# Kernel optimization log

Hardware: AMD Instinct MI355X
Metric: run time of the kernel (lower is better)

The kernel has to match this reference:

```python
import jax, jax.numpy as jnp
import numpy as np

DIMS = 3; B = 256; N = 256; K = 16; HID = 64; INC = 64; F = 64; EPG = 8192; DEPTH = 3
EPS = 1e-15


def setup_inputs() -> dict:
    key = jax.random.key(0)
    ks = jax.random.split(key, 16)
    E = B * EPG
    g = jnp.repeat(jnp.arange(B), EPG)
    row = (g * N + jax.random.randint(ks[0], (E,), 0, N)).astype(jnp.int32)
    col = (g * N + jax.random.randint(ks[1], (E,), 0, N)).astype(jnp.int32)
    edge_index = jnp.stack([row, col])
    edge_attr = jax.random.uniform(ks[2], (E, DIMS), dtype=jnp.float32)
    x = jax.random.normal(ks[3], (B * N, INC), dtype=jnp.float32)
    x_to_pool = jax.random.normal(ks[4], (B * N, F * DIMS), dtype=jnp.float32)
    batch = jnp.repeat(jnp.arange(B), N).astype(jnp.int32)
    def w(k, shape, fan):
        return (jax.random.normal(k, shape, dtype=jnp.float32) / np.float32(np.sqrt(fan)))
    return dict(
        x=x, edge_attr=edge_attr, x_to_pool=x_to_pool,
        Wm0=w(ks[5], (DIMS, INC, HID), INC), Ws0=w(ks[6], (DIMS, INC, HID), INC), b0=jnp.zeros((DIMS, HID), jnp.float32),
        Wm1=w(ks[7], (DIMS, HID, HID), HID), Ws1=w(ks[8], (DIMS, HID, HID), HID), b1=jnp.zeros((DIMS, HID), jnp.float32),
        Wm2=w(ks[9], (DIMS, HID, K), HID), Ws2=w(ks[10], (DIMS, HID, K), HID), b2=jnp.zeros((DIMS, K), jnp.float32),
        fcW1=w(ks[11], (HID * (DEPTH - 1) + K, 50), HID * (DEPTH - 1) + K), fcb1=jnp.zeros((50,), jnp.float32),
        fcW2=w(ks[12], (50, K), 50), fcb2=jnp.zeros((K,), jnp.float32),
        edge_index=edge_index, batch=batch,
    )


def reference(x, edge_attr, x_to_pool, Wm0, Ws0, b0, Wm1, Ws1, b1, Wm2, Ws2, b2,
              fcW1, fcb1, fcW2, fcb2, edge_index, batch):
    row, col = edge_index[0], edge_index[1]
    n_total = B * N

    # ---- batch_to_adj: scatter edge list into dense (dims, B, N, N) adjacency ----
    ge, rl, cl = row // N, row % N, col % N
    adj = jnp.zeros((DIMS, B, N, N), x.dtype).at[:, ge, rl, cl].add(edge_attr.T)

    # ---- ParallelResGraphConv: per-dim edge-weighted graph conv stack ----
    def gconv(h, we, Wm, Ws, b):
        agg = jax.ops.segment_sum(we[:, None] * h[col], row, num_segments=n_total)
        return jax.nn.relu(agg @ Wm + h @ Ws + b)

    assignments = []
    for d in range(DIMS):  # small fixed loop over parallel streams
        we = edge_attr[:, d]
        h0 = gconv(x, we, Wm0[d], Ws0[d], b0[d])
        h1 = gconv(h0, we, Wm1[d], Ws1[d], b1[d])
        h2 = gconv(h1, we, Wm2[d], Ws2[d], b2[d])
        conv_out = jnp.concatenate([h0, h1, h2], axis=-1)  # [BN, HID*2+K]
        logits = (conv_out @ fcW1 + fcb1) @ fcW2 + fcb2     # shared pool_fc
        assignments.append(logits)
    s = jax.nn.softmax(jnp.stack(assignments).reshape(DIMS, B, N, K), axis=-1)

    # ---- losses: modularity (edge gather) + entropy ----
    a_flat = s.reshape(DIMS, n_total, K)
    mod = jnp.float32(0.0)
    for d in range(DIMS):
        diff = a_flat[d, row] - a_flat[d, col]
        mod = mod + jnp.mean(edge_attr[:, d] * jnp.sum(diff * diff, axis=-1))
    ent = jnp.mean(jnp.sum(-s * jnp.log(s + EPS), axis=-1))
    loss = mod + ent

    # ---- DiffPool-style pooling ----
    xr = x_to_pool.reshape(n_total, F, DIMS)
    xr = jnp.transpose(xr, (2, 0, 1)).reshape(DIMS, B, N, F)
    px = jnp.einsum('dbnk,dbnf->dbkf', s, xr)
    tmp = jnp.einsum('dbnk,dbnm->dbkm', s, adj)
    padj = jnp.einsum('dbkm,dbml->dbkl', tmp, s)
    scale = jnp.float32(K / N)
    px = jnp.transpose(px, (1, 2, 3, 0)).reshape(B * K, F, DIMS) * scale
    padj = padj * (scale * scale)

    # ---- adj_to_tg_batch: dense pooled adjacency back to edge list (fixed shapes) ----
    rows = jnp.repeat(jnp.arange(K), K)
    cols = jnp.tile(jnp.arange(K), K)
    off = (jnp.arange(B) * K)[:, None]
    pei = jnp.stack([(off + rows[None, :]).reshape(-1), (off + cols[None, :]).reshape(-1)]).astype(jnp.int32)
    pea = jax.lax.stop_gradient(jnp.transpose(padj, (1, 2, 3, 0)).reshape(-1, DIMS))  # detach_pool=True
    pbatch = jnp.repeat(jnp.arange(B), K).astype(jnp.int32)
    return (px, pei, pea, pbatch, loss, s)
```

## Files before the change

### kernel.cpp

```cpp
#include <hip/hip_runtime.h>

#define DIMS 3
#define NB 256
#define NN 256
#define KK 16
#define HID 64
#define EPG 8192
#define NTOT (NB*NN)
#define NE (NB*EPG)

#define PX_OFF   0
#define PEI_OFF  786432
#define PEA_OFF  917504
#define PB_OFF   1114112
#define LOSS_OFF 1118208
#define S_OFF    1118209

#define WREC_WS  0
#define CLREC_WS 25165824
#define IPTR_WS  27262976
#define ENT_WS   27526144
#define MOD_WS   27529216
#define WC_WS    27532288
#define BC_WS    27541504

__global__ void fc_combine(const float* __restrict__ fcW1, const float* __restrict__ fcb1,
                           const float* __restrict__ fcW2, const float* __restrict__ fcb2,
                           float* __restrict__ wc, float* __restrict__ bc)
{
    const int t = threadIdx.x;
    for (int idx = t; idx < 144 * 16; idx += 256) {
        const int i = idx >> 4, k = idx & 15;
        float s = 0.f;
        for (int q = 0; q < 50; ++q) s += fcW1[i * 50 + q] * fcW2[q * 16 + k];
        wc[idx] = s;
    }
    if (t < 16) {
        float s = fcb2[t];
        for (int q = 0; q < 50; ++q) s += fcb1[q] * fcW2[q * 16 + t];
        bc[t] = s;
    }
}

#define HSTR 132
#define PSTR 129
__launch_bounds__(256)
__global__ void csr_build(const int* __restrict__ edge_index,
                          const float* __restrict__ edge_attr,
                          float* __restrict__ wrec, unsigned char* __restrict__ clrec,
                          int* __restrict__ indptr)
{
    __shared__ unsigned char  h[256 * HSTR];
    __shared__ unsigned short po[256 * PSTR];
    __shared__ int sc[256];
    const int b = blockIdx.x;
    const int t = threadIdx.x;
    const int* rowp = edge_index + (size_t)b * EPG;
    const int* colp = edge_index + (size_t)NB * EPG + (size_t)b * EPG;

    for (int i = t; i < 256 * HSTR / 4; i += 256) ((unsigned int*)h)[i] = 0u;
    __syncthreads();

    if (t < 128) {
        #pragma unroll 4
        for (int j = 0; j < 64; ++j) {
            const int r = rowp[t + 128 * j] & (NN - 1);
            h[r * HSTR + t]++;
        }
    }
    __syncthreads();

    int tot;
    {
        int s = 0;
        const unsigned int* hr = (const unsigned int*)(h + t * HSTR);
        #pragma unroll
        for (int c4 = 0; c4 < HSTR / 4; ++c4) {
            const unsigned int v = hr[c4];
            s += (v & 255) + ((v >> 8) & 255) + ((v >> 16) & 255) + (v >> 24);
        }
        tot = s;
        sc[t] = s;
    }
    __syncthreads();
    for (int ofs = 1; ofs < 256; ofs <<= 1) {
        int v = (t >= ofs) ? sc[t - ofs] : 0;
        __syncthreads();
        sc[t] += v;
        __syncthreads();
    }
    const int start = sc[t] - tot;
    indptr[b * 257 + t] = start;
    if (t == 255) indptr[b * 257 + 256] = EPG;

    {
        int run = start;
        #pragma unroll 4
        for (int c = 0; c < 128; ++c) {
            po[t * PSTR + c] = (unsigned short)run;
            run += h[t * HSTR + c];
        }
    }
    __syncthreads();

    if (t < 128) {
        const float* eap = edge_attr + (size_t)b * EPG * 3;
        float* w0 = wrec + (size_t)b * EPG;
        float* w1 = wrec + (size_t)NB * EPG + (size_t)b * EPG;
        float* w2 = wrec + 2 * (size_t)NB * EPG + (size_t)b * EPG;
        unsigned char* cdst = clrec + (size_t)b * EPG;
        #pragma unroll 2
        for (int j = 0; j < 64; ++j) {
            const int e = t + 128 * j;
            const int r = rowp[e] & (NN - 1);
            const int cl = colp[e] & (NN - 1);
            const int dest = po[r * PSTR + t]++;
            w0[dest] = eap[e * 3 + 0];
            w1[dest] = eap[e * 3 + 1];
            w2[dest] = eap[e * 3 + 2];
            cdst[dest] = (unsigned char)cl;
        }
    }
}

template<int OUTW, bool IS_L2>
__device__ __forceinline__ void layer_step(
    int rp, int o, int fr, int fkq, int js0, int je0, int je1,
    const float* __restrict__ wp, const unsigned char* __restrict__ clp,
    const float* __restrict__ Wm, const float* __restrict__ Ws,
    const float* __restrict__ bias, const float* __restrict__ wc,
    float4* hb4, float* p)
{
    constexpr int NCO = OUTW / 8;
    const int r0 = rp * 2, r1 = r0 + 1;
    const int b0 = r0 * 16, s0 = r0 & 15;
    const int b1 = r1 * 16, s1 = r1 & 15;
    const int c0 = o, c1 = o + 8;

    float ga0[8], ga1[8];
    #pragma unroll
    for (int u = 0; u < 8; ++u) { ga0[u] = 0.f; ga1[u] = 0.f; }
    for (int j = js0; j < je0; ++j) {
        const int cl = clp[j];
        const float w = wp[j];
        const int cb = cl * 16, cs = cl & 15;
        const float4 ha = hb4[cb + (c0 ^ cs)];
        const float4 hb = hb4[cb + (c1 ^ cs)];
        ga0[0] += w * ha.x; ga0[1] += w * ha.y; ga0[2] += w * ha.z; ga0[3] += w * ha.w;
        ga0[4] += w * hb.x; ga0[5] += w * hb.y; ga0[6] += w * hb.z; ga0[7] += w * hb.w;
    }
    for (int j = je0; j < je1; ++j) {
        const int cl = clp[j];
        const float w = wp[j];
        const int cb = cl * 16, cs = cl & 15;
        const float4 ha = hb4[cb + (c0 ^ cs)];
        const float4 hb = hb4[cb + (c1 ^ cs)];
        ga1[0] += w * ha.x; ga1[1] += w * ha.y; ga1[2] += w * ha.z; ga1[3] += w * ha.w;
        ga1[4] += w * hb.x; ga1[5] += w * hb.y; ga1[6] += w * hb.z; ga1[7] += w * hb.w;
    }

    const int jA = o * 4;
    const int jB = o * 4 + 32;
    const int j0L2 = o * NCO;
    float acc0[NCO == 8 ? 8 : 2], acc1[NCO == 8 ? 8 : 2];
    if constexpr (NCO == 8) {
        const float4 bv0 = *(const float4*)(bias + jA);
        const float4 bv1 = *(const float4*)(bias + jB);
        acc0[0]=bv0.x; acc0[1]=bv0.y; acc0[2]=bv0.z; acc0[3]=bv0.w;
        acc0[4]=bv1.x; acc0[5]=bv1.y; acc0[6]=bv1.z; acc0[7]=bv1.w;
        #pragma unroll
        for (int u = 0; u < 8; ++u) acc1[u] = acc0[u];
    } else {
        acc0[0] = bias[j0L2]; acc0[1] = bias[j0L2 + 1];
        acc1[0] = acc0[0];    acc1[1] = acc0[1];
    }
    #pragma unroll 1
    for (int ic = 0; ic < 16; ++ic) {
        const float4 h40 = hb4[b0 + (ic ^ s0)];
        const float4 h41 = hb4[b1 + (ic ^ s1)];
        const float hv0[4] = {h40.x, h40.y, h40.z, h40.w};
        const float hv1[4] = {h41.x, h41.y, h41.z, h41.w};
        #pragma unroll
        for (int u = 0; u < 4; ++u) {
            const float* wr = Ws + (ic * 4 + u) * OUTW;
            const float a0 = hv0[u], a1 = hv1[u];
            if constexpr (NCO == 8) {
                const float4 wa = *(const float4*)(wr + jA);
                const float4 wb = *(const float4*)(wr + jB);
                acc0[0]+=a0*wa.x; acc0[1]+=a0*wa.y; acc0[2]+=a0*wa.z; acc0[3]+=a0*wa.w;
                acc0[4]+=a0*wb.x; acc0[5]+=a0*wb.y; acc0[6]+=a0*wb.z; acc0[7]+=a0*wb.w;
                acc1[0]+=a1*wa.x; acc1[1]+=a1*wa.y; acc1[2]+=a1*wa.z; acc1[3]+=a1*wa.w;
                acc1[4]+=a1*wb.x; acc1[5]+=a1*wb.y; acc1[6]+=a1*wb.z; acc1[7]+=a1*wb.w;
            } else {
                const float2 w2 = *(const float2*)(wr + j0L2);
                acc0[0]+=a0*w2.x; acc0[1]+=a0*w2.y;
                acc1[0]+=a1*w2.x; acc1[1]+=a1*w2.y;
            }
        }
    }
    __syncthreads();

    {
        float4 v;
        v.x = ga0[0]; v.y = ga0[1]; v.z = ga0[2]; v.w = ga0[3]; hb4[b0 + (c0 ^ s0)] = v;
        v.x = ga0[4]; v.y = ga0[5]; v.z = ga0[6]; v.w = ga0[7]; hb4[b0 + (c1 ^ s0)] = v;
        v.x = ga1[0]; v.y = ga1[1]; v.z = ga1[2]; v.w = ga1[3]; hb4[b1 + (c0 ^ s1)] = v;
        v.x = ga1[4]; v.y = ga1[5]; v.z = ga1[6]; v.w = ga1[7]; hb4[b1 + (c1 ^ s1)] = v;
    }
    __syncthreads();

    #pragma unroll 1
    for (int ic = 0; ic < 16; ++ic) {
        const float4 a40 = hb4[b0 + (ic ^ s0)];
        const float4 a41 = hb4[b1 + (ic ^ s1)];
        const float av0[4] = {a40.x, a40.y, a40.z, a40.w};
        const float av1[4] = {a41.x, a41.y, a41.z, a41.w};
        #pragma unroll
        for (int u = 0; u < 4; ++u) {
            const float* wr = Wm + (ic * 4 + u) * OUTW;
            const float a0 = av0[u], a1 = av1[u];
            if constexpr (NCO == 8) {
                const float4 wa = *(const float4*)(wr + jA);
                const float4 wb = *(const float4*)(wr + jB);
                acc0[0]+=a0*wa.x; acc0[1]+=a0*wa.y; acc0[2]+=a0*wa.z; acc0[3]+=a0*wa.w;
                acc0[4]+=a0*wb.x; acc0[5]+=a0*wb.y; acc0[6]+=a0*wb.z; acc0[7]+=a0*wb.w;
                acc1[0]+=a1*wa.x; acc1[1]+=a1*wa.y; acc1[2]+=a1*wa.z; acc1[3]+=a1*wa.w;
                acc1[4]+=a1*wb.x; acc1[5]+=a1*wb.y; acc1[6]+=a1*wb.z; acc1[7]+=a1*wb.w;
            } else {
                const float2 w2 = *(const float2*)(wr + j0L2);
                acc0[0]+=a0*w2.x; acc0[1]+=a0*w2.y;
                acc1[0]+=a1*w2.x; acc1[1]+=a1*w2.y;
            }
        }
    }
    #pragma unroll
    for (int jj = 0; jj < NCO; ++jj) {
        acc0[jj] = fmaxf(acc0[jj], 0.f);
        acc1[jj] = fmaxf(acc1[jj], 0.f);
    }
    __syncthreads();

    if constexpr (!IS_L2) {
        float4 v;
        v.x = acc0[0]; v.y = acc0[1]; v.z = acc0[2]; v.w = acc0[3]; hb4[b0 + (c0 ^ s0)] = v;
        v.x = acc0[4]; v.y = acc0[5]; v.z = acc0[6]; v.w = acc0[7]; hb4[b0 + (c1 ^ s0)] = v;
        v.x = acc1[0]; v.y = acc1[1]; v.z = acc1[2]; v.w = acc1[3]; hb4[b1 + (c0 ^ s1)] = v;
        v.x = acc1[4]; v.y = acc1[5]; v.z = acc1[6]; v.w = acc1[7]; hb4[b1 + (c1 ^ s1)] = v;
    } else {
        float* hbf = (float*)hb4;
        const int cc = o >> 1, off = (o & 1) * 2;
        float* p0 = hbf + (b0 + (cc ^ s0)) * 4 + off;
        float* p1 = hbf + (b1 + (cc ^ s1)) * 4 + off;
        p0[0] = acc0[0]; p0[1] = acc0[1];
        p1[0] = acc1[0]; p1[1] = acc1[1];
    }
    __syncthreads();

    {
        const int rb = fr * 16, rs = fr & 15;
        if constexpr (!IS_L2) {
            #pragma unroll 2
            for (int c4 = 0; c4 < 16; ++c4) {
                const float4 v4 = hb4[rb + (c4 ^ rs)];
                const float vv[4] = {v4.x, v4.y, v4.z, v4.w};
                #pragma unroll
                for (int e = 0; e < 4; ++e) {
                    const float4 w4 = *(const float4*)(wc + (c4 * 4 + e) * 16 + fkq * 4);
                    p[0] += vv[e] * w4.x; p[1] += vv[e] * w4.y;
                    p[2] += vv[e] * w4.z; p[3] += vv[e] * w4.w;
                }
            }
        } else {
            #pragma unroll 2
            for (int c4 = 0; c4 < 4; ++c4) {
                const float4 v4 = hb4[rb + (c4 ^ rs)];
                const float vv[4] = {v4.x, v4.y, v4.z, v4.w};
                #pragma unroll
                for (int e = 0; e < 4; ++e) {
                    const float4 w4 = *(const float4*)(wc + (c4 * 4 + e) * 16 + fkq * 4);
                    p[0] += vv[e] * w4.x; p[1] += vv[e] * w4.y;
                    p[2] += vv[e] * w4.z; p[3] += vv[e] * w4.w;
                }
            }
        }
    }
}

__launch_bounds__(1024)
__global__ void gconv_kernel(
    const float* __restrict__ x,
    const float* __restrict__ Wm0, const float* __restrict__ Ws0, const float* __restrict__ b0,
    const float* __restrict__ Wm1, const float* __restrict__ Ws1, const float* __restrict__ b1,
    const float* __restrict__ Wm2, const float* __restrict__ Ws2, const float* __restrict__ b2,
    const float* __restrict__ wcomb, const float* __restrict__ bcomb,
    const float* __restrict__ wrec, const unsigned char* __restrict__ clrec,
    const int* __restrict__ indptr,
    float* __restrict__ out, float* __restrict__ entpart)
{
    __shared__ float4 hb4[4096];
    __shared__ float  red[16];
    const int t = threadIdx.x;
    const int bid = blockIdx.x;
    const int d = bid >> 8;
    const int b = bid & (NB - 1);
    const int rp = t >> 3;
    const int o = t & 7;
    const int fr = t >> 2;
    const int fkq = t & 3;
    const int lane = t & 63;
    const int wave = t >> 6;

    {
        const float4* xv = (const float4*)(x + (size_t)b * NN * HID);
        #pragma unroll
        for (int it = 0; it < 4; ++it) {
            const int idx = t + it * 1024;
            const int nrow = idx >> 4, c = idx & 15;
            hb4[nrow * 16 + (c ^ (nrow & 15))] = xv[idx];
        }
    }
    float p[4] = {0.f, 0.f, 0.f, 0.f};
    __syncthreads();

    const float* wp = wrec + (size_t)d * NB * EPG + (size_t)b * EPG;
    const unsigned char* clp = clrec + (size_t)b * EPG;
    const int js0 = indptr[b * 257 + rp * 2];
    const int je0 = indptr[b * 257 + rp * 2 + 1];
    const int je1 = indptr[b * 257 + rp * 2 + 2];

    layer_step<64, false>(rp, o, fr, fkq, js0, je0, je1, wp, clp, Wm0 + d*HID*HID,
                          Ws0 + d*HID*HID, b0 + d*HID, wcomb,          hb4, p);
    layer_step<64, false>(rp, o, fr, fkq, js0, je0, je1, wp, clp, Wm1 + d*HID*HID,
                          Ws1 + d*HID*HID, b1 + d*HID, wcomb + 64*16,  hb4, p);
    layer_step<16, true >(rp, o, fr, fkq, js0, je0, je1, wp, clp, Wm2 + d*HID*KK,
                          Ws2 + d*HID*KK,  b2 + d*KK,  wcomb + 128*16, hb4, p);

    __syncthreads();
    {
        float* hbf = (float*)hb4;
        float* dst = hbf + fr * 17 + fkq * 4;
        dst[0] = p[0]; dst[1] = p[1]; dst[2] = p[2]; dst[3] = p[3];
    }
    __syncthreads();

    float ent_local = 0.f;
    if (t < 256) {
        const int rr = t;
        const float* Lr = (const float*)hb4 + rr * 17;
        float logits[KK];
        #pragma unroll
        for (int k = 0; k < KK; ++k) logits[k] = Lr[k] + bcomb[k];
        float m = logits[0];
        #pragma unroll
        for (int k = 1; k < KK; ++k) m = fmaxf(m, logits[k]);
        float sum = 0.f, sv[KK];
        #pragma unroll
        for (int k = 0; k < KK; ++k) { sv[k] = expf(logits[k] - m); sum += sv[k]; }
        const float inv = 1.f / sum;
        float4* sp4 = (float4*)(out + S_OFF + ((size_t)(d * NB + b) * NN + rr) * KK);
        #pragma unroll
        for (int q4 = 0; q4 < 4; ++q4) {
            float4 v;
            const float s0 = sv[q4*4+0] * inv, s1 = sv[q4*4+1] * inv;
            const float s2 = sv[q4*4+2] * inv, s3 = sv[q4*4+3] * inv;
            v.x = s0; v.y = s1; v.z = s2; v.w = s3;
            sp4[q4] = v;
            ent_local -= s0 * logf(s0 + 1e-15f) + s1 * logf(s1 + 1e-15f)
                       + s2 * logf(s2 + 1e-15f) + s3 * logf(s3 + 1e-15f);
        }
    }
    #pragma unroll
    for (int off = 32; off; off >>= 1) ent_local += __shfl_down(ent_local, off);
    if (lane == 0) red[wave] = ent_local;
    __syncthreads();
    if (t == 0) {
        float s = 0.f;
        #pragma unroll
        for (int w = 0; w < 16; ++w) s += red[w];
        entpart[bid] = s;
    }
}

#define SSTR 20
__launch_bounds__(256)
__global__ void pool_kernel(
    const float* __restrict__ x_to_pool,
    const float* __restrict__ wrec, const unsigned char* __restrict__ clrec,
    const int* __restrict__ indptr,
    const float* __restrict__ out_s, float* __restrict__ out, float* __restrict__ modpart)
{
    __shared__ float sl[NN * SSTR];
    __shared__ float gl[NN * SSTR];
    __shared__ float padjw[4 * 256];
    __shared__ float red[4];
    const int t = threadIdx.x;
    const int bid = blockIdx.x;
    const int d = bid >> 8;
    const int b = bid & (NB - 1);
    const int lane = t & 63;
    const int wave = t >> 6;

    {
        const float4* sp4 = (const float4*)(out_s + S_OFF + (size_t)(d * NB + b) * NN * KK);
        #pragma unroll
        for (int it = 0; it < 4; ++it) {
            const int idx = t + it * 256;
            const int nrow = idx >> 2, c = idx & 3;
            *(float4*)(sl + nrow * SSTR + c * 4) = sp4[idx];
        }
    }
    __syncthreads();

    const float* wp = wrec + (size_t)d * NB * EPG + (size_t)b * EPG;
    const unsigned char* clp = clrec + (size_t)b * EPG;
    const int js = indptr[b * 257 + t];
    const int je = indptr[b * 257 + t + 1];
    float sr[16];
    {
        #pragma unroll
        for (int c = 0; c < 4; ++c) {
            const float4 v = *(const float4*)(sl + t * SSTR + c * 4);
            sr[c*4+0] = v.x; sr[c*4+1] = v.y; sr[c*4+2] = v.z; sr[c*4+3] = v.w;
        }
    }
    float g[16];
    #pragma unroll
    for (int k = 0; k < 16; ++k) g[k] = 0.f;
    float modacc = 0.f;
    for (int j = js; j < je; ++j) {
        const int cl = clp[j];
        const float w = wp[j];
        const float* srow = sl + cl * SSTR;
        float ss = 0.f;
        #pragma unroll
        for (int c = 0; c < 4; ++c) {
            const float4 sv = *(const float4*)(srow + c * 4);
            g[c*4+0] += w * sv.x; g[c*4+1] += w * sv.y;
            g[c*4+2] += w * sv.z; g[c*4+3] += w * sv.w;
            const float d0 = sr[c*4+0] - sv.x, d1 = sr[c*4+1] - sv.y;
            const float d2 = sr[c*4+2] - sv.z, d3 = sr[c*4+3] - sv.w;
            ss += d0*d0 + d1*d1 + d2*d2 + d3*d3;
        }
        modacc += w * ss;
    }
    {
        #pragma unroll
        for (int c = 0; c < 4; ++c) {
            float4 v; v.x = g[c*4+0]; v.y = g[c*4+1]; v.z = g[c*4+2]; v.w = g[c*4+3];
            *(float4*)(gl + t * SSTR + c * 4) = v;
        }
    }
    __syncthreads();

    {
        const int k = t & 15, lg = (t >> 4) & 3;
        float p0 = 0.f, p1 = 0.f, p2 = 0.f, p3 = 0.f;
        const int r0 = wave * 64;
        for (int rr = r0; rr < r0 + 64; ++rr) {
            const float sk = sl[rr * SSTR + k];
            const float4 g4 = *(const float4*)(gl + rr * SSTR + lg * 4);
            p0 += sk * g4.x; p1 += sk * g4.y; p2 += sk * g4.z; p3 += sk * g4.w;
        }
        float* pw = padjw + wave * 256 + k * 16 + lg * 4;
        pw[0] = p0; pw[1] = p1; pw[2] = p2; pw[3] = p3;
    }

    {
        const int f = t & 63;
        const int kg = t >> 6;
        float xa0 = 0.f, xa1 = 0.f, xa2 = 0.f, xa3 = 0.f;
        const float* xp = x_to_pool + (size_t)b * NN * (64 * DIMS) + f * DIMS + d;
        #pragma unroll 4
        for (int nn2 = 0; nn2 < NN; ++nn2) {
            const float xv = xp[(size_t)nn2 * (64 * DIMS)];
            const float4 s4 = *(const float4*)(sl + nn2 * SSTR + kg * 4);
            xa0 += xv * s4.x; xa1 += xv * s4.y; xa2 += xv * s4.z; xa3 += xv * s4.w;
        }
        const float sc = 1.f / 16.f;
        out[PX_OFF + ((size_t)((b * KK + kg * 4 + 0) * 64) + f) * DIMS + d] = xa0 * sc;
        out[PX_OFF + ((size_t)((b * KK + kg * 4 + 1) * 64) + f) * DIMS + d] = xa1 * sc;
        out[PX_OFF + ((size_t)((b * KK + kg * 4 + 2) * 64) + f) * DIMS + d] = xa2 * sc;
        out[PX_OFF + ((size_t)((b * KK + kg * 4 + 3) * 64) + f) * DIMS + d] = xa3 * sc;
    }

    #pragma unroll
    for (int off = 32; off; off >>= 1) modacc += __shfl_down(modacc, off);
    if (lane == 0) red[wave] = modacc;
    __syncthreads();
    if (t == 0) modpart[bid] = red[0] + red[1] + red[2] + red[3];

    {
        const float v = (padjw[t] + padjw[256 + t] + padjw[512 + t] + padjw[768 + t]) * (1.f / 256.f);
        out[PEA_OFF + (size_t)((b * KK + (t >> 4)) * KK + (t & 15)) * DIMS + d] = v;
    }
}

__global__ void aux_kernel(float* __restrict__ out)
{
    const int idx = blockIdx.x * 256 + threadIdx.x;
    if (idx < 2 * NTOT) {
        const int r = idx & (NTOT - 1);
        const int bb = r >> 8;
        const int j = r & 255;
        const int v = (idx < NTOT) ? (bb * KK + (j >> 4)) : (bb * KK + (j & 15));
        out[PEI_OFF + idx] = (float)v;
    } else if (idx < 2 * NTOT + NB * KK) {
        const int i = idx - 2 * NTOT;
        out[PB_OFF + i] = (float)(i >> 4);
    }
}

__global__ void loss_kernel(const float* __restrict__ entpart,
                            const float* __restrict__ modpart,
                            float* __restrict__ out)
{
    const int tid = threadIdx.x;
    float e = 0.f, m = 0.f;
    for (int i = tid; i < DIMS * NB; i += 256) { e += entpart[i]; m += modpart[i]; }
    #pragma unroll
    for (int off = 32; off; off >>= 1) { e += __shfl_down(e, off); m += __shfl_down(m, off); }
    __shared__ float er[4], mr[4];
    const int wave = tid >> 6, lane = tid & 63;
    if (lane == 0) { er[wave] = e; mr[wave] = m; }
    __syncthreads();
    if (tid == 0) {
        const float es = er[0] + er[1] + er[2] + er[3];
        const float ms = mr[0] + mr[1] + mr[2] + mr[3];
        out[LOSS_OFF] = ms / (float)NE + es / (float)(DIMS * NTOT);
    }
}

extern "C" void kernel_launch(void* const* d_in, const int* in_sizes, int n_in,
                              void* d_out, int out_size, void* d_ws, size_t ws_size,
                              hipStream_t stream)
{
    const float* x         = (const float*)d_in[0];
    const float* edge_attr = (const float*)d_in[1];
    const float* x_to_pool = (const float*)d_in[2];
    const float* Wm0 = (const float*)d_in[3];
    const float* Ws0 = (const float*)d_in[4];
    const float* b0  = (const float*)d_in[5];
    const float* Wm1 = (const float*)d_in[6];
    const float* Ws1 = (const float*)d_in[7];
    const float* b1  = (const float*)d_in[8];
    const float* Wm2 = (const float*)d_in[9];
    const float* Ws2 = (const float*)d_in[10];
    const float* b2  = (const float*)d_in[11];
    const float* fcW1= (const float*)d_in[12];
    const float* fcb1= (const float*)d_in[13];
    const float* fcW2= (const float*)d_in[14];
    const float* fcb2= (const float*)d_in[15];
    const int* edge_index = (const int*)d_in[16];
    float* out = (float*)d_out;
    char* ws = (char*)d_ws;
    float*         wrec  = (float*)(ws + WREC_WS);
    unsigned char* clrec = (unsigned char*)(ws + CLREC_WS);
    int*           iptr  = (int*)(ws + IPTR_WS);
    float*         entpart = (float*)(ws + ENT_WS);
    float*         modpart = (float*)(ws + MOD_WS);
    float*         wc    = (float*)(ws + WC_WS);
    float*         bc    = (float*)(ws + BC_WS);

    csr_build<<<dim3(NB), dim3(256), 0, stream>>>(edge_index, edge_attr, wrec, clrec, iptr);
    fc_combine<<<dim3(1), dim3(256), 0, stream>>>(fcW1, fcb1, fcW2, fcb2, wc, bc);
    gconv_kernel<<<dim3(DIMS * NB), dim3(1024), 0, stream>>>(
        x, Wm0, Ws0, b0, Wm1, Ws1, b1, Wm2, Ws2, b2,
        wc, bc, wrec, clrec, iptr, out, entpart);
    pool_kernel<<<dim3(DIMS * NB), dim3(256), 0, stream>>>(
        x_to_pool, wrec, clrec, iptr, out, out, modpart);
    aux_kernel<<<dim3((2 * NTOT + NB * KK + 255) / 256), dim3(256), 0, stream>>>(out);
    loss_kernel<<<dim3(1), dim3(256), 0, stream>>>(entpart, modpart, out);
}
```

Before: 578.8 us.

## Fuse pooling stage into gconv kernel, keeping assignments in shared memory

The separate pool_kernel is folded into the tail of gconv_kernel. The softmax assignments are kept in LDS instead of being re-read from global memory, and the pooling work is redistributed across 1024 threads. Aggregation now uses 4 threads per row, padj uses 4 row groups, and the px reduction is split into 4 row groups combined through shared memory. This removes a kernel launch and a global round trip of s. The cost is extra work and barriers at the end of a high-occupancy 1024-thread kernel.

Measured after the change: 575.6 us. Within noise of the previous version (-0.6%).

```diff
diff --git a/kernel.cpp b/kernel.cpp
--- a/kernel.cpp
+++ b/kernel.cpp
@@ -23,6 +23,13 @@
 #define MOD_WS   27529216
 #define WC_WS    27532288
 #define BC_WS    27541504
+
+#define SL_OFF   0
+#define GL_OFF   5120
+#define PXP_OFF  10240
+#define PJW_OFF  14336
+#define MRED_OFF 15360
+#define ERED_OFF 15380
 
 __global__ void fc_combine(const float* __restrict__ fcW1, const float* __restrict__ fcb1,
                            const float* __restrict__ fcW2, const float* __restrict__ fcb2,
@@ -289,16 +296,17 @@
 __launch_bounds__(1024)
 __global__ void gconv_kernel(
     const float* __restrict__ x,
+    const float* __restrict__ x_to_pool,
     const float* __restrict__ Wm0, const float* __restrict__ Ws0, const float* __restrict__ b0,
     const float* __restrict__ Wm1, const float* __restrict__ Ws1, const float* __restrict__ b1,
     const float* __restrict__ Wm2, const float* __restrict__ Ws2, const float* __restrict__ b2,
     const float* __restrict__ wcomb, const float* __restrict__ bcomb,
     const float* __restrict__ wrec, const unsigned char* __restrict__ clrec,
     const int* __restrict__ indptr,
-    float* __restrict__ out, float* __restrict__ entpart)
+    float* __restrict__ out, float* __restrict__ entpart, float* __restrict__ modpart)
 {
     __shared__ float4 hb4[4096];
-    __shared__ float  red[16];
+    float* hbf = (float*)hb4;
     const int t = threadIdx.x;
     const int bid = blockIdx.x;
     const int d = bid >> 8;
@@ -324,9 +332,10 @@
 
     const float* wp = wrec + (size_t)d * NB * EPG + (size_t)b * EPG;
     const unsigned char* clp = clrec + (size_t)b * EPG;
-    const int js0 = indptr[b * 257 + rp * 2];
-    const int je0 = indptr[b * 257 + rp * 2 + 1];
-    const int je1 = indptr[b * 257 + rp * 2 + 2];
+    const int* ipb = indptr + b * 257;
+    const int js0 = ipb[rp * 2];
+    const int je0 = ipb[rp * 2 + 1];
+    const int je1 = ipb[rp * 2 + 2];
 
     layer_step<64, false>(rp, o, fr, fkq, js0, je0, je1, wp, clp, Wm0 + d*HID*HID,
                           Ws0 + d*HID*HID, b0 + d*HID, wcomb,          hb4, p);
@@ -337,8 +346,7 @@
 
     __syncthreads();
     {
-        float* hbf = (float*)hb4;
-        float* dst = hbf + fr * 17 + fkq * 4;
+        float* dst = hbf + SL_OFF + fr * 20 + fkq * 4;
         dst[0] = p[0]; dst[1] = p[1]; dst[2] = p[2]; dst[3] = p[3];
     }
     __syncthreads();
@@ -346,7 +354,7 @@
     float ent_local = 0.f;
     if (t < 256) {
         const int rr = t;
-        const float* Lr = (const float*)hb4 + rr * 17;
+        float* Lr = hbf + SL_OFF + rr * 20;
         float logits[KK];
         #pragma unroll
         for (int k = 0; k < KK; ++k) logits[k] = Lr[k] + bcomb[k];
@@ -365,133 +373,91 @@
             const float s2 = sv[q4*4+2] * inv, s3 = sv[q4*4+3] * inv;
             v.x = s0; v.y = s1; v.z = s2; v.w = s3;
             sp4[q4] = v;
+            *(float4*)(Lr + q4 * 4) = v;
             ent_local -= s0 * logf(s0 + 1e-15f) + s1 * logf(s1 + 1e-15f)
                        + s2 * logf(s2 + 1e-15f) + s3 * logf(s3 + 1e-15f);
         }
     }
     #pragma unroll
     for (int off = 32; off; off >>= 1) ent_local += __shfl_down(ent_local, off);
-    if (lane == 0) red[wave] = ent_local;
+    if (lane == 0) hbf[ERED_OFF + wave] = ent_local;
     __syncthreads();
     if (t == 0) {
         float s = 0.f;
         #pragma unroll
-        for (int w = 0; w < 16; ++w) s += red[w];
+        for (int w = 0; w < 16; ++w) s += hbf[ERED_OFF + w];
         entpart[bid] = s;
     }
-}
-
-#define SSTR 20
-__launch_bounds__(256)
-__global__ void pool_kernel(
-    const float* __restrict__ x_to_pool,
-    const float* __restrict__ wrec, const unsigned char* __restrict__ clrec,
-    const int* __restrict__ indptr,
-    const float* __restrict__ out_s, float* __restrict__ out, float* __restrict__ modpart)
-{
-    __shared__ float sl[NN * SSTR];
-    __shared__ float gl[NN * SSTR];
-    __shared__ float padjw[4 * 256];
-    __shared__ float red[4];
-    const int t = threadIdx.x;
-    const int bid = blockIdx.x;
-    const int d = bid >> 8;
-    const int b = bid & (NB - 1);
-    const int lane = t & 63;
-    const int wave = t >> 6;
-
-    {
-        const float4* sp4 = (const float4*)(out_s + S_OFF + (size_t)(d * NB + b) * NN * KK);
-        #pragma unroll
-        for (int it = 0; it < 4; ++it) {
-            const int idx = t + it * 256;
-            const int nrow = idx >> 2, c = idx & 3;
-            *(float4*)(sl + nrow * SSTR + c * 4) = sp4[idx];
-        }
-    }
-    __syncthreads();
-
-    const float* wp = wrec + (size_t)d * NB * EPG + (size_t)b * EPG;
-    const unsigned char* clp = clrec + (size_t)b * EPG;
-    const int js = indptr[b * 257 + t];
-    const int je = indptr[b * 257 + t + 1];
-    float sr[16];
-    {
-        #pragma unroll
-        for (int c = 0; c < 4; ++c) {
-            const float4 v = *(const float4*)(sl + t * SSTR + c * 4);
-            sr[c*4+0] = v.x; sr[c*4+1] = v.y; sr[c*4+2] = v.z; sr[c*4+3] = v.w;
-        }
-    }
-    float g[16];
-    #pragma unroll
-    for (int k = 0; k < 16; ++k) g[k] = 0.f;
-    float modacc = 0.f;
-    for (int j = js; j < je; ++j) {
-        const int cl = clp[j];
-        const float w = wp[j];
-        const float* srow = sl + cl * SSTR;
-        float ss = 0.f;
-        #pragma unroll
-        for (int c = 0; c < 4; ++c) {
-            const float4 sv = *(const float4*)(srow + c * 4);
-            g[c*4+0] += w * sv.x; g[c*4+1] += w * sv.y;
-            g[c*4+2] += w * sv.z; g[c*4+3] += w * sv.w;
-            const float d0 = sr[c*4+0] - sv.x, d1 = sr[c*4+1] - sv.y;
-            const float d2 = sr[c*4+2] - sv.z, d3 = sr[c*4+3] - sv.w;
-            ss += d0*d0 + d1*d1 + d2*d2 + d3*d3;
-        }
-        modacc += w * ss;
-    }
-    {
-        #pragma unroll
-        for (int c = 0; c < 4; ++c) {
-            float4 v; v.x = g[c*4+0]; v.y = g[c*4+1]; v.z = g[c*4+2]; v.w = g[c*4+3];
-            *(float4*)(gl + t * SSTR + c * 4) = v;
-        }
-    }
-    __syncthreads();
-
-    {
-        const int k = t & 15, lg = (t >> 4) & 3;
-        float p0 = 0.f, p1 = 0.f, p2 = 0.f, p3 = 0.f;
-        const int r0 = wave * 64;
-        for (int rr = r0; rr < r0 + 64; ++rr) {
-            const float sk = sl[rr * SSTR + k];
-            const float4 g4 = *(const float4*)(gl + rr * SSTR + lg * 4);
-            p0 += sk * g4.x; p1 += sk * g4.y; p2 += sk * g4.z; p3 += sk * g4.w;
-        }
-        float* pw = padjw + wave * 256 + k * 16 + lg * 4;
-        pw[0] = p0; pw[1] = p1; pw[2] = p2; pw[3] = p3;
-    }
-
-    {
-        const int f = t & 63;
-        const int kg = t >> 6;
+
+    {
+        const int pr = t >> 2, pkq = t & 3;
+        const int pjs = ipb[pr], pje = ipb[pr + 1];
+        const float4 sq = *(const float4*)(hbf + SL_OFF + pr * 20 + pkq * 4);
+        float g0 = 0.f, g1 = 0.f, g2 = 0.f, g3 = 0.f;
+        float modp = 0.f;
+        for (int j = pjs; j < pje; ++j) {
+            const int cl = clp[j];
+            const float w = wp[j];
+            const float4 sc4 = *(const float4*)(hbf + SL_OFF + cl * 20 + pkq * 4);
+            g0 += w * sc4.x; g1 += w * sc4.y; g2 += w * sc4.z; g3 += w * sc4.w;
+            const float d0 = sq.x - sc4.x, d1 = sq.y - sc4.y;
+            const float d2 = sq.z - sc4.z, d3 = sq.w - sc4.w;
+            modp += w * (d0*d0 + d1*d1 + d2*d2 + d3*d3);
+        }
+        float4 gv; gv.x = g0; gv.y = g1; gv.z = g2; gv.w = g3;
+        *(float4*)(hbf + GL_OFF + pr * 20 + pkq * 4) = gv;
+        #pragma unroll
+        for (int off = 32; off; off >>= 1) modp += __shfl_down(modp, off);
+        if (lane == 0) hbf[MRED_OFF + wave] = modp;
+    }
+    __syncthreads();
+    if (t == 0) {
+        float s = 0.f;
+        #pragma unroll
+        for (int w = 0; w < 16; ++w) s += hbf[MRED_OFF + w];
+        modpart[bid] = s;
+    }
+
+    {
+        const int q = t >> 8, kl = t & 255;
+        const int k = kl >> 4, l = kl & 15;
+        float acc = 0.f;
+        const int r0 = q * 64;
+        #pragma unroll 4
+        for (int r = r0; r < r0 + 64; ++r)
+            acc += hbf[SL_OFF + r * 20 + k] * hbf[GL_OFF + r * 20 + l];
+        hbf[PJW_OFF + q * 256 + kl] = acc;
+    }
+
+    {
+        const int rg = t >> 8, kg = (t >> 6) & 3, f = t & 63;
+        const float* xp = x_to_pool + (size_t)b * NN * (64 * DIMS) + f * DIMS + d;
         float xa0 = 0.f, xa1 = 0.f, xa2 = 0.f, xa3 = 0.f;
-        const float* xp = x_to_pool + (size_t)b * NN * (64 * DIMS) + f * DIMS + d;
+        const int n0 = rg * 64;
         #pragma unroll 4
-        for (int nn2 = 0; nn2 < NN; ++nn2) {
-            const float xv = xp[(size_t)nn2 * (64 * DIMS)];
-            const float4 s4 = *(const float4*)(sl + nn2 * SSTR + kg * 4);
+        for (int n = n0; n < n0 + 64; ++n) {
+            const float xv = xp[(size_t)n * (64 * DIMS)];
+            const float4 s4 = *(const float4*)(hbf + SL_OFF + n * 20 + kg * 4);
             xa0 += xv * s4.x; xa1 += xv * s4.y; xa2 += xv * s4.z; xa3 += xv * s4.w;
         }
-        const float sc = 1.f / 16.f;
-        out[PX_OFF + ((size_t)((b * KK + kg * 4 + 0) * 64) + f) * DIMS + d] = xa0 * sc;
-        out[PX_OFF + ((size_t)((b * KK + kg * 4 + 1) * 64) + f) * DIMS + d] = xa1 * sc;
-        out[PX_OFF + ((size_t)((b * KK + kg * 4 + 2) * 64) + f) * DIMS + d] = xa2 * sc;
-        out[PX_OFF + ((size_t)((b * KK + kg * 4 + 3) * 64) + f) * DIMS + d] = xa3 * sc;
-    }
-
-    #pragma unroll
-    for (int off = 32; off; off >>= 1) modacc += __shfl_down(modacc, off);
-    if (lane == 0) red[wave] = modacc;
-    __syncthreads();
-    if (t == 0) modpart[bid] = red[0] + red[1] + red[2] + red[3];
-
-    {
-        const float v = (padjw[t] + padjw[256 + t] + padjw[512 + t] + padjw[768 + t]) * (1.f / 256.f);
+        float4 v; v.x = xa0; v.y = xa1; v.z = xa2; v.w = xa3;
+        *(float4*)(hbf + PXP_OFF + ((rg * 4 + kg) * 64 + f) * 4) = v;
+    }
+    __syncthreads();
+
+    if (t < 256) {
+        const float v = (hbf[PJW_OFF + t] + hbf[PJW_OFF + 256 + t]
+                       + hbf[PJW_OFF + 512 + t] + hbf[PJW_OFF + 768 + t]) * (1.f / 256.f);
         out[PEA_OFF + (size_t)((b * KK + (t >> 4)) * KK + (t & 15)) * DIMS + d] = v;
+    }
+    {
+        const int k = t >> 6, f = t & 63;
+        const int kg = k >> 2, e = k & 3;
+        float s = 0.f;
+        #pragma unroll
+        for (int rg = 0; rg < 4; ++rg)
+            s += hbf[PXP_OFF + ((rg * 4 + kg) * 64 + f) * 4 + e];
+        out[PX_OFF + ((size_t)((b * KK + k) * 64) + f) * DIMS + d] = s * (1.f / 16.f);
     }
 }
 
@@ -564,10 +530,8 @@
     csr_build<<<dim3(NB), dim3(256), 0, stream>>>(edge_index, edge_attr, wrec, clrec, iptr);
     fc_combine<<<dim3(1), dim3(256), 0, stream>>>(fcW1, fcb1, fcW2, fcb2, wc, bc);
     gconv_kernel<<<dim3(DIMS * NB), dim3(1024), 0, stream>>>(
-        x, Wm0, Ws0, b0, Wm1, Ws1, b1, Wm2, Ws2, b2,
-        wc, bc, wrec, clrec, iptr, out, entpart);
-    pool_kernel<<<dim3(DIMS * NB), dim3(256), 0, stream>>>(
-        x_to_pool, wrec, clrec, iptr, out, out, modpart);
+        x, x_to_pool, Wm0, Ws0, b0, Wm1, Ws1, b1, Wm2, Ws2, b2,
+        wc, bc, wrec, clrec, iptr, out, entpart, modpart);
     aux_kernel<<<dim3((2 * NTOT + NB * KK + 255) / 256), dim3(256), 0, stream>>>(out);
     loss_kernel<<<dim3(1), dim3(256), 0, stream>>>(entpart, modpart, out);
 }
```
